# Kernel optimization log

Measured on AMD Instinct MI355X. Metric: run time of the kernel, lower is better.

The kernel has to match this reference:

```python
import jax, jax.numpy as jnp
import numpy as np

NUM_HEADS = 12


def setup_inputs() -> dict:
    key = jax.random.key(0)
    k1, k2, k3 = jax.random.split(key, 3)
    B, S, D = 2, 2048, 768
    x = jax.random.normal(k1, (B, S, D), dtype=jnp.float32)
    # torch Linear init: normal(std=0.002) weights, zero bias; stored as [in, out]
    W_qkv = jax.random.normal(k2, (D, 3 * D), dtype=jnp.float32) * 0.002
    b_qkv = jnp.zeros((3 * D,), dtype=jnp.float32)
    W_vw = jax.random.normal(k3, (D, D), dtype=jnp.float32) * 0.002
    b_vw = jnp.zeros((D,), dtype=jnp.float32)
    mask = jnp.ones((B, S), dtype=jnp.int32)  # padding mask, all valid
    return {"x": x, "W_qkv": W_qkv, "b_qkv": b_qkv, "W_vw": W_vw, "b_vw": b_vw, "mask": mask}


def reference(x, W_qkv, b_qkv, W_vw, b_vw, mask):
    B, S, D = x.shape
    H = NUM_HEADS
    Dh = D // H
    qkv = (x @ W_qkv + b_qkv).reshape(B, S, 3, H, Dh)
    q, k, v = qkv[:, :, 0], qkv[:, :, 1], qkv[:, :, 2]
    # [B, H, S, S] attention scores (full matrix, as in original)
    w = jnp.einsum('bshd,bzhd->bhsz', q, k)
    w = w / jnp.sqrt(jnp.asarray(Dh, dtype=x.dtype))  # scale=True
    # log-mask trick: padding mask [B,1,1,S] * causal tril [1,1,S,S]
    causal = jnp.tril(jnp.ones((S, S), dtype=x.dtype))
    wholemask = mask.astype(x.dtype)[:, None, None, :] * causal[None, None]
    w = w + jnp.log(wholemask)
    w = jax.nn.softmax(w, axis=-1)
    vw = jnp.einsum('bhsz,bzhd->bshd', w, v).reshape(B, S, D)
    return vw @ W_vw + b_vw
```

## Files before the change

### kernel.cpp

```cpp
#include <hip/hip_runtime.h>
#include <cmath>
#include <cstddef>

#define B_    2
#define S_    2048
#define D_    768
#define H_    12
#define DH_   64
#define NQKV_ 2304

typedef __attribute__((ext_vector_type(8))) short  short8;
typedef __attribute__((ext_vector_type(4))) float  floatx4;

__device__ __forceinline__ unsigned short f2bf(float f) {
    union { float f; unsigned u; } v; v.f = f;
    unsigned r = v.u + 0x7fffu + ((v.u >> 16) & 1u);
    return (unsigned short)(r >> 16);
}

__device__ __forceinline__ void stage16(const unsigned short* g, unsigned short* ldsbase, int lane) {
#if __has_builtin(__builtin_amdgcn_global_load_lds)
    __builtin_amdgcn_global_load_lds(
        (const __attribute__((address_space(1))) unsigned int*)g,
        (__attribute__((address_space(3))) unsigned int*)ldsbase, 16, 0, 0);
#else
    *(short8*)(ldsbase + lane * 8) = *(const short8*)g;
#endif
}

__global__ void cvt_x_kernel(const float* __restrict__ x, unsigned short* __restrict__ xb)
{
    int i = (blockIdx.x * 256 + threadIdx.x) * 8;
    float4 a = *(const float4*)(x + i);
    float4 b = *(const float4*)(x + i + 4);
    short8 v;
    v[0] = (short)f2bf(a.x); v[1] = (short)f2bf(a.y);
    v[2] = (short)f2bf(a.z); v[3] = (short)f2bf(a.w);
    v[4] = (short)f2bf(b.x); v[5] = (short)f2bf(b.y);
    v[6] = (short)f2bf(b.z); v[7] = (short)f2bf(b.w);
    *(short8*)(xb + i) = v;
}

__global__ void cvt_w_kernel(const float* __restrict__ Wq, const float* __restrict__ Wv,
                             unsigned short* __restrict__ WqT, unsigned short* __restrict__ WvT)
{
    const int z = blockIdx.z;
    const int N = z ? D_ : NQKV_;
    if ((int)blockIdx.x * 32 >= N) return;
    const float* W = z ? Wv : Wq;
    unsigned short* WT = z ? WvT : WqT;

    __shared__ float t[32][33];
    const int tx = threadIdx.x, ty = threadIdx.y;
    const int n0 = blockIdx.x * 32, k0 = blockIdx.y * 32;
    #pragma unroll
    for (int i = 0; i < 4; ++i)
        t[ty + i * 8][tx] = W[(size_t)(k0 + ty + i * 8) * N + n0 + tx];
    __syncthreads();
    #pragma unroll
    for (int i = 0; i < 4; ++i)
        WT[(size_t)(n0 + ty + i * 8) * 768 + k0 + tx] = f2bf(t[tx][ty + i * 8]);
}

__global__ void vt_kernel(const unsigned short* __restrict__ V, unsigned short* __restrict__ VT)
{
    __shared__ unsigned short t[64][72];
    const int bh = blockIdx.x, s0 = blockIdx.y * 64;
    const unsigned short* src = V + ((size_t)bh * S_ + s0) * DH_;
    const int r = threadIdx.x >> 3, c = (threadIdx.x & 7) * 8;
    #pragma unroll
    for (int it = 0; it < 2; ++it)
        *(short8*)&t[r + it * 32][c] = *(const short8*)(src + (size_t)(r + it * 32) * DH_ + c);
    __syncthreads();
    #pragma unroll
    for (int it = 0; it < 2; ++it) {
        int d = r + it * 32;
        short8 v;
        #pragma unroll
        for (int i = 0; i < 8; ++i) v[i] = (short)t[c + i][d];
        *(short8*)(VT + ((size_t)bh * DH_ + d) * S_ + s0 + c) = v;
    }
}

__global__ __launch_bounds__(256, 2)
void mm_qkv_kernel(const unsigned short* __restrict__ A, const unsigned short* __restrict__ BT,
                   const float* __restrict__ bias,
                   unsigned short* __restrict__ Qo, unsigned short* __restrict__ Ko,
                   unsigned short* __restrict__ Vo)
{
    __shared__ unsigned short As[128][32];
    __shared__ unsigned short Bs[128][32];
    const int tid = threadIdx.x;
    const int wid = tid >> 6, lane = tid & 63;
    const int q = lane >> 4, ln = lane & 15;
    const int wm = (wid & 1) * 64, wn = (wid >> 1) * 64;
    const int m0 = blockIdx.y * 128, n0 = blockIdx.x * 128;
    const int lrow = wid * 16 + (lane >> 2);
    const int lcol = (lane & 3) * 8;
    const unsigned short* Ag = A  + (size_t)(m0 + lrow) * 768 + lcol;
    const unsigned short* Bg = BT + (size_t)(n0 + lrow) * 768 + lcol;

    floatx4 acc[4][4] = {};
    for (int k0 = 0; k0 < 768; k0 += 32) {
        __syncthreads();
        stage16(Ag + k0,            &As[wid * 16][0],      lane);
        stage16(Ag + k0 + 64 * 768, &As[64 + wid * 16][0], lane);
        stage16(Bg + k0,            &Bs[wid * 16][0],      lane);
        stage16(Bg + k0 + 64 * 768, &Bs[64 + wid * 16][0], lane);
        __syncthreads();
        short8 af[4], bf[4];
        #pragma unroll
        for (int mt = 0; mt < 4; ++mt) af[mt] = *(const short8*)&As[wm + mt * 16 + ln][q * 8];
        #pragma unroll
        for (int nt = 0; nt < 4; ++nt) bf[nt] = *(const short8*)&Bs[wn + nt * 16 + ln][q * 8];
        #pragma unroll
        for (int mt = 0; mt < 4; ++mt)
            #pragma unroll
            for (int nt = 0; nt < 4; ++nt)
                acc[mt][nt] = __builtin_amdgcn_mfma_f32_16x16x32_bf16(af[mt], bf[nt], acc[mt][nt], 0, 0, 0);
    }

    const int t = n0 / 768;
    unsigned short* __restrict__ dst = (t == 0) ? Qo : ((t == 1) ? Ko : Vo);
    const int colb = n0 - t * 768 + wn;
    float bv[4];
    #pragma unroll
    for (int nt = 0; nt < 4; ++nt) bv[nt] = bias[n0 + wn + nt * 16 + ln];
    #pragma unroll
    for (int mt = 0; mt < 4; ++mt)
        #pragma unroll
        for (int r = 0; r < 4; ++r) {
            int row = m0 + wm + mt * 16 + q * 4 + r;
            int bb = row >> 11, s = row & 2047;
            #pragma unroll
            for (int nt = 0; nt < 4; ++nt) {
                int col = colb + nt * 16 + ln;
                int h = col >> 6, d = col & 63;
                dst[((size_t)(bb * H_ + h) * S_ + s) * DH_ + d] = f2bf(acc[mt][nt][r] + bv[nt]);
            }
        }
}

__global__ __launch_bounds__(256, 2)
void flash6_kernel(const unsigned short* __restrict__ Qg, const unsigned short* __restrict__ Kg,
                   const unsigned short* __restrict__ VTg, const int* __restrict__ mask,
                   unsigned short* __restrict__ VW)
{
    __shared__ unsigned short Pl[4][32][40];
    __shared__ float Ol[32][68];
    __shared__ float li_s[4][32];

    const int tid = threadIdx.x;
    const int wid = tid >> 6, lane = tid & 63;
    const int q = lane >> 4, ln = lane & 15;
    const int bh = blockIdx.x % 24;
    const int qt = 63 - blockIdx.x / 24;
    const int b = bh / H_, h = bh % H_;
    const int r0 = qt * 32;

    const unsigned short* Qb = Qg  + (size_t)bh * S_ * DH_;
    const unsigned short* Kb = Kg  + (size_t)bh * S_ * DH_;
    const unsigned short* Vt = VTg + (size_t)bh * DH_ * S_;
    const int* mb = mask + b * S_;

    short8 qf[2][2];
    #pragma unroll
    for (int mt = 0; mt < 2; ++mt)
        #pragma unroll
        for (int kk = 0; kk < 2; ++kk)
            qf[mt][kk] = *(const short8*)(Qb + (size_t)(r0 + mt * 16 + ln) * DH_ + kk * 32 + q * 8);

    floatx4 o[2][4] = {};
    float li[2][4] = {};
    const float SC = 0.125f * 1.4426950408889634f;
    const int T = qt + 1;

    for (int t = wid; t < T; t += 4) {
        const int z0 = t * 32;

        short8 kb[2][2];
        #pragma unroll
        for (int nt = 0; nt < 2; ++nt)
            #pragma unroll
            for (int kk = 0; kk < 2; ++kk)
                kb[nt][kk] = *(const short8*)(Kb + (size_t)(z0 + nt * 16 + ln) * DH_ + kk * 32 + q * 8);

        floatx4 s[2][2] = {};
        #pragma unroll
        for (int mt = 0; mt < 2; ++mt)
            #pragma unroll
            for (int nt = 0; nt < 2; ++nt) {
                s[mt][nt] = __builtin_amdgcn_mfma_f32_16x16x32_bf16(qf[mt][0], kb[nt][0], s[mt][nt], 0, 0, 0);
                s[mt][nt] = __builtin_amdgcn_mfma_f32_16x16x32_bf16(qf[mt][1], kb[nt][1], s[mt][nt], 0, 0, 0);
            }

        short8 vb[4];
        #pragma unroll
        for (int dt = 0; dt < 4; ++dt)
            vb[dt] = *(const short8*)(Vt + (size_t)(dt * 16 + ln) * S_ + z0 + q * 8);

        float mv[2];
        #pragma unroll
        for (int nt = 0; nt < 2; ++nt) mv[nt] = mb[z0 + nt * 16 + ln] ? 1.0f : 0.0f;

        const bool diag = (z0 + 31 > r0);
        #pragma unroll
        for (int mt = 0; mt < 2; ++mt)
            #pragma unroll
            for (int nt = 0; nt < 2; ++nt) {
                int z = z0 + nt * 16 + ln;
                #pragma unroll
                for (int r = 0; r < 4; ++r) {
                    float p = exp2f(s[mt][nt][r] * SC) * mv[nt];
                    if (diag) {
                        int row = r0 + mt * 16 + q * 4 + r;
                        if (z > row) p = 0.0f;
                    }
                    li[mt][r] += p;
                    Pl[wid][mt * 16 + q * 4 + r][nt * 16 + ln] = f2bf(p);
                }
            }

        #pragma unroll
        for (int mt = 0; mt < 2; ++mt) {
            short8 a = *(const short8*)&Pl[wid][mt * 16 + ln][q * 8];
            #pragma unroll
            for (int dt = 0; dt < 4; ++dt)
                o[mt][dt] = __builtin_amdgcn_mfma_f32_16x16x32_bf16(a, vb[dt], o[mt][dt], 0, 0, 0);
        }
    }

    #pragma unroll
    for (int mt = 0; mt < 2; ++mt)
        #pragma unroll
        for (int r = 0; r < 4; ++r) {
            float v = li[mt][r];
            v += __shfl_xor(v, 1);
            v += __shfl_xor(v, 2);
            v += __shfl_xor(v, 4);
            v += __shfl_xor(v, 8);
            li[mt][r] = v;
        }

    #pragma unroll
    for (int w = 0; w < 4; ++w) {
        if (wid == w) {
            #pragma unroll
            for (int mt = 0; mt < 2; ++mt)
                #pragma unroll
                for (int r = 0; r < 4; ++r) {
                    int row = mt * 16 + q * 4 + r;
                    #pragma unroll
                    for (int dt = 0; dt < 4; ++dt) {
                        if (w == 0) Ol[row][dt * 16 + ln]  = o[mt][dt][r];
                        else        Ol[row][dt * 16 + ln] += o[mt][dt][r];
                    }
                    if (ln == 0) li_s[w][row] = li[mt][r];
                }
        }
        __syncthreads();
    }

    {
        int row = tid >> 3, c = (tid & 7) * 8;
        float inv = 1.0f / (li_s[0][row] + li_s[1][row] + li_s[2][row] + li_s[3][row]);
        short8 ov;
        #pragma unroll
        for (int i = 0; i < 8; ++i) ov[i] = (short)f2bf(Ol[row][c + i] * inv);
        *(short8*)(VW + ((size_t)b * S_ + r0 + row) * D_ + h * DH_ + c) = ov;
    }
}

__global__ __launch_bounds__(256, 2)
void mm_proj_kernel(const unsigned short* __restrict__ A, const unsigned short* __restrict__ BT,
                    const float* __restrict__ bias, float* __restrict__ C)
{
    __shared__ unsigned short As[128][32];
    __shared__ unsigned short Bs[64][32];
    const int tid = threadIdx.x;
    const int wid = tid >> 6, lane = tid & 63;
    const int q = lane >> 4, ln = lane & 15;
    const int wm = (wid & 1) * 64, wn = (wid >> 1) * 32;
    const int m0 = blockIdx.y * 128, n0 = blockIdx.x * 64;
    const int lrow = wid * 16 + (lane >> 2);
    const int lcol = (lane & 3) * 8;
    const unsigned short* Ag = A  + (size_t)(m0 + lrow) * 768 + lcol;
    const unsigned short* Bg = BT + (size_t)(n0 + lrow) * 768 + lcol;

    floatx4 acc[4][2] = {};
    for (int k0 = 0; k0 < 768; k0 += 32) {
        __syncthreads();
        stage16(Ag + k0,            &As[wid * 16][0],      lane);
        stage16(Ag + k0 + 64 * 768, &As[64 + wid * 16][0], lane);
        stage16(Bg + k0,            &Bs[wid * 16][0],      lane);
        __syncthreads();
        short8 af[4], bf[2];
        #pragma unroll
        for (int mt = 0; mt < 4; ++mt) af[mt] = *(const short8*)&As[wm + mt * 16 + ln][q * 8];
        #pragma unroll
        for (int nt = 0; nt < 2; ++nt) bf[nt] = *(const short8*)&Bs[wn + nt * 16 + ln][q * 8];
        #pragma unroll
        for (int mt = 0; mt < 4; ++mt)
            #pragma unroll
            for (int nt = 0; nt < 2; ++nt)
                acc[mt][nt] = __builtin_amdgcn_mfma_f32_16x16x32_bf16(af[mt], bf[nt], acc[mt][nt], 0, 0, 0);
    }

    float bv[2];
    #pragma unroll
    for (int nt = 0; nt < 2; ++nt) bv[nt] = bias[n0 + wn + nt * 16 + ln];
    #pragma unroll
    for (int mt = 0; mt < 4; ++mt)
        #pragma unroll
        for (int r = 0; r < 4; ++r) {
            size_t row = (size_t)m0 + wm + mt * 16 + q * 4 + r;
            #pragma unroll
            for (int nt = 0; nt < 2; ++nt)
                C[row * D_ + n0 + wn + nt * 16 + ln] = acc[mt][nt][r] + bv[nt];
        }
}

extern "C" void kernel_launch(void* const* d_in, const int* in_sizes, int n_in,
                              void* d_out, int out_size, void* d_ws, size_t ws_size,
                              hipStream_t stream)
{
    (void)in_sizes; (void)n_in; (void)out_size; (void)ws_size;
    const float* x    = (const float*)d_in[0];
    const float* Wqkv = (const float*)d_in[1];
    const float* bqkv = (const float*)d_in[2];
    const float* Wvw  = (const float*)d_in[3];
    const float* bvw  = (const float*)d_in[4];
    const int*   mask = (const int*)d_in[5];
    float* out = (float*)d_out;

    const size_t XN  = (size_t)B_ * S_ * D_;
    unsigned short* ws  = (unsigned short*)d_ws;
    unsigned short* xb  = ws;
    unsigned short* WqT = xb  + XN;
    unsigned short* WvT = WqT + (size_t)NQKV_ * D_;
    unsigned short* Qb  = WvT + (size_t)D_ * D_;
    unsigned short* Kb  = Qb + XN;
    unsigned short* Vb  = Kb + XN;
    unsigned short* VbT = Vb + XN;
    unsigned short* VW  = VbT + XN;

    cvt_x_kernel<<<dim3(XN / (256 * 8)), 256, 0, stream>>>(x, xb);
    cvt_w_kernel<<<dim3(NQKV_ / 32, D_ / 32, 2), dim3(32, 8), 0, stream>>>(Wqkv, Wvw, WqT, WvT);
    mm_qkv_kernel<<<dim3(NQKV_ / 128, (B_ * S_) / 128), 256, 0, stream>>>(xb, WqT, bqkv, Qb, Kb, Vb);
    vt_kernel<<<dim3(B_ * H_, S_ / 64), 256, 0, stream>>>(Vb, VbT);
    flash6_kernel<<<dim3(24 * 64), 256, 0, stream>>>(Qb, Kb, VbT, mask, VW);
    mm_proj_kernel<<<dim3(D_ / 64, (B_ * S_) / 128), 256, 0, stream>>>(VW, WvT, bvw, out);
}
```

Baseline: 187.9 us.

## Pair causal query tiles per block, fold softmax scale into Q, add fast path

The attention kernel now processes two query tiles per block (tile i and tile 63-i), so every block does the same amount of causal work and the grid is halved. The softmax scale times log2(e) is folded into Q at the QKV projection epilogue, which removes a multiply per score. A fast path skips the per-element mask and causal checks for fully valid off-diagonal tiles, s_setprio hints are placed around the MFMA groups, and f2bf now uses the HIP bf16 intrinsic. Halving the grid leaves fewer blocks to hide latency, and rounding Q after scaling changes numerics slightly.

```diff
diff --git a/kernel.cpp b/kernel.cpp
--- a/kernel.cpp
+++ b/kernel.cpp
@@ -1,4 +1,5 @@
 #include <hip/hip_runtime.h>
+#include <hip/hip_bf16.h>
 #include <cmath>
 #include <cstddef>
 
@@ -13,9 +14,9 @@
 typedef __attribute__((ext_vector_type(4))) float  floatx4;
 
 __device__ __forceinline__ unsigned short f2bf(float f) {
-    union { float f; unsigned u; } v; v.f = f;
-    unsigned r = v.u + 0x7fffu + ((v.u >> 16) & 1u);
-    return (unsigned short)(r >> 16);
+    union { __hip_bfloat16 h; unsigned short u; } cv;
+    cv.h = __float2bfloat16(f);
+    return cv.u;
 }
 
 __device__ __forceinline__ void stage16(const unsigned short* g, unsigned short* ldsbase, int lane) {
@@ -122,6 +123,7 @@
 
     const int t = n0 / 768;
     unsigned short* __restrict__ dst = (t == 0) ? Qo : ((t == 1) ? Ko : Vo);
+    const float qscale = (t == 0) ? 0.18033688011112042f : 1.0f;
     const int colb = n0 - t * 768 + wn;
     float bv[4];
     #pragma unroll
@@ -136,13 +138,13 @@
             for (int nt = 0; nt < 4; ++nt) {
                 int col = colb + nt * 16 + ln;
                 int h = col >> 6, d = col & 63;
-                dst[((size_t)(bb * H_ + h) * S_ + s) * DH_ + d] = f2bf(acc[mt][nt][r] + bv[nt]);
+                dst[((size_t)(bb * H_ + h) * S_ + s) * DH_ + d] = f2bf((acc[mt][nt][r] + bv[nt]) * qscale);
             }
         }
 }
 
 __global__ __launch_bounds__(256, 2)
-void flash6_kernel(const unsigned short* __restrict__ Qg, const unsigned short* __restrict__ Kg,
+void flash8_kernel(const unsigned short* __restrict__ Qg, const unsigned short* __restrict__ Kg,
                    const unsigned short* __restrict__ VTg, const int* __restrict__ mask,
                    unsigned short* __restrict__ VW)
 {
@@ -154,120 +156,143 @@
     const int wid = tid >> 6, lane = tid & 63;
     const int q = lane >> 4, ln = lane & 15;
     const int bh = blockIdx.x % 24;
-    const int qt = 63 - blockIdx.x / 24;
+    const int pix = blockIdx.x / 24;
     const int b = bh / H_, h = bh % H_;
-    const int r0 = qt * 32;
 
     const unsigned short* Qb = Qg  + (size_t)bh * S_ * DH_;
     const unsigned short* Kb = Kg  + (size_t)bh * S_ * DH_;
     const unsigned short* Vt = VTg + (size_t)bh * DH_ * S_;
     const int* mb = mask + b * S_;
 
-    short8 qf[2][2];
-    #pragma unroll
-    for (int mt = 0; mt < 2; ++mt)
-        #pragma unroll
-        for (int kk = 0; kk < 2; ++kk)
-            qf[mt][kk] = *(const short8*)(Qb + (size_t)(r0 + mt * 16 + ln) * DH_ + kk * 32 + q * 8);
-
-    floatx4 o[2][4] = {};
-    float li[2][4] = {};
-    const float SC = 0.125f * 1.4426950408889634f;
-    const int T = qt + 1;
-
-    for (int t = wid; t < T; t += 4) {
-        const int z0 = t * 32;
-
-        short8 kb[2][2];
-        #pragma unroll
-        for (int nt = 0; nt < 2; ++nt)
+    for (int half = 0; half < 2; ++half) {
+        const int qt = half ? (63 - pix) : pix;
+        const int r0 = qt * 32;
+        const int T = qt + 1;
+
+        short8 qf[2][2];
+        #pragma unroll
+        for (int mt = 0; mt < 2; ++mt)
             #pragma unroll
             for (int kk = 0; kk < 2; ++kk)
-                kb[nt][kk] = *(const short8*)(Kb + (size_t)(z0 + nt * 16 + ln) * DH_ + kk * 32 + q * 8);
-
-        floatx4 s[2][2] = {};
+                qf[mt][kk] = *(const short8*)(Qb + (size_t)(r0 + mt * 16 + ln) * DH_ + kk * 32 + q * 8);
+
+        floatx4 o[2][4] = {};
+        float li[2][4] = {};
+
+        for (int t = wid; t < T; t += 4) {
+            const int z0 = t * 32;
+
+            short8 kb[2][2];
+            #pragma unroll
+            for (int nt = 0; nt < 2; ++nt)
+                #pragma unroll
+                for (int kk = 0; kk < 2; ++kk)
+                    kb[nt][kk] = *(const short8*)(Kb + (size_t)(z0 + nt * 16 + ln) * DH_ + kk * 32 + q * 8);
+
+            short8 vb[4];
+            #pragma unroll
+            for (int dt = 0; dt < 4; ++dt)
+                vb[dt] = *(const short8*)(Vt + (size_t)(dt * 16 + ln) * S_ + z0 + q * 8);
+
+            const int m0i = mb[z0 + ln];
+            const int m1i = mb[z0 + 16 + ln];
+
+            floatx4 s[2][2] = {};
+            __builtin_amdgcn_s_setprio(1);
+            #pragma unroll
+            for (int mt = 0; mt < 2; ++mt)
+                #pragma unroll
+                for (int nt = 0; nt < 2; ++nt) {
+                    s[mt][nt] = __builtin_amdgcn_mfma_f32_16x16x32_bf16(qf[mt][0], kb[nt][0], s[mt][nt], 0, 0, 0);
+                    s[mt][nt] = __builtin_amdgcn_mfma_f32_16x16x32_bf16(qf[mt][1], kb[nt][1], s[mt][nt], 0, 0, 0);
+                }
+            __builtin_amdgcn_s_setprio(0);
+
+            const bool diag = (z0 + 31 > r0);
+            if (__all(m0i && m1i) && !diag) {
+                #pragma unroll
+                for (int mt = 0; mt < 2; ++mt)
+                    #pragma unroll
+                    for (int nt = 0; nt < 2; ++nt)
+                        #pragma unroll
+                        for (int r = 0; r < 4; ++r) {
+                            float p = exp2f(s[mt][nt][r]);
+                            li[mt][r] += p;
+                            Pl[wid][mt * 16 + q * 4 + r][nt * 16 + ln] = f2bf(p);
+                        }
+            } else {
+                float mv[2];
+                mv[0] = m0i ? 1.0f : 0.0f;
+                mv[1] = m1i ? 1.0f : 0.0f;
+                #pragma unroll
+                for (int mt = 0; mt < 2; ++mt)
+                    #pragma unroll
+                    for (int nt = 0; nt < 2; ++nt) {
+                        int z = z0 + nt * 16 + ln;
+                        #pragma unroll
+                        for (int r = 0; r < 4; ++r) {
+                            float p = exp2f(s[mt][nt][r]) * mv[nt];
+                            if (diag) {
+                                int row = r0 + mt * 16 + q * 4 + r;
+                                if (z > row) p = 0.0f;
+                            }
+                            li[mt][r] += p;
+                            Pl[wid][mt * 16 + q * 4 + r][nt * 16 + ln] = f2bf(p);
+                        }
+                    }
+            }
+
+            #pragma unroll
+            for (int mt = 0; mt < 2; ++mt) {
+                short8 a = *(const short8*)&Pl[wid][mt * 16 + ln][q * 8];
+                __builtin_amdgcn_s_setprio(1);
+                #pragma unroll
+                for (int dt = 0; dt < 4; ++dt)
+                    o[mt][dt] = __builtin_amdgcn_mfma_f32_16x16x32_bf16(a, vb[dt], o[mt][dt], 0, 0, 0);
+                __builtin_amdgcn_s_setprio(0);
+            }
+        }
+
         #pragma unroll
         for (int mt = 0; mt < 2; ++mt)
             #pragma unroll
-            for (int nt = 0; nt < 2; ++nt) {
-                s[mt][nt] = __builtin_amdgcn_mfma_f32_16x16x32_bf16(qf[mt][0], kb[nt][0], s[mt][nt], 0, 0, 0);
-                s[mt][nt] = __builtin_amdgcn_mfma_f32_16x16x32_bf16(qf[mt][1], kb[nt][1], s[mt][nt], 0, 0, 0);
-            }
-
-        short8 vb[4];
-        #pragma unroll
-        for (int dt = 0; dt < 4; ++dt)
-            vb[dt] = *(const short8*)(Vt + (size_t)(dt * 16 + ln) * S_ + z0 + q * 8);
-
-        float mv[2];
-        #pragma unroll
-        for (int nt = 0; nt < 2; ++nt) mv[nt] = mb[z0 + nt * 16 + ln] ? 1.0f : 0.0f;
-
-        const bool diag = (z0 + 31 > r0);
-        #pragma unroll
-        for (int mt = 0; mt < 2; ++mt)
-            #pragma unroll
-            for (int nt = 0; nt < 2; ++nt) {
-                int z = z0 + nt * 16 + ln;
-                #pragma unroll
-                for (int r = 0; r < 4; ++r) {
-                    float p = exp2f(s[mt][nt][r] * SC) * mv[nt];
-                    if (diag) {
-                        int row = r0 + mt * 16 + q * 4 + r;
-                        if (z > row) p = 0.0f;
+            for (int r = 0; r < 4; ++r) {
+                float v = li[mt][r];
+                v += __shfl_xor(v, 1);
+                v += __shfl_xor(v, 2);
+                v += __shfl_xor(v, 4);
+                v += __shfl_xor(v, 8);
+                li[mt][r] = v;
+            }
+
+        #pragma unroll
+        for (int w = 0; w < 4; ++w) {
+            if (wid == w) {
+                #pragma unroll
+                for (int mt = 0; mt < 2; ++mt)
+                    #pragma unroll
+                    for (int r = 0; r < 4; ++r) {
+                        int row = mt * 16 + q * 4 + r;
+                        #pragma unroll
+                        for (int dt = 0; dt < 4; ++dt) {
+                            if (w == 0) Ol[row][dt * 16 + ln]  = o[mt][dt][r];
+                            else        Ol[row][dt * 16 + ln] += o[mt][dt][r];
+                        }
+                        if (ln == 0) li_s[w][row] = li[mt][r];
                     }
-                    li[mt][r] += p;
-                    Pl[wid][mt * 16 + q * 4 + r][nt * 16 + ln] = f2bf(p);
-                }
-            }
-
-        #pragma unroll
-        for (int mt = 0; mt < 2; ++mt) {
-            short8 a = *(const short8*)&Pl[wid][mt * 16 + ln][q * 8];
-            #pragma unroll
-            for (int dt = 0; dt < 4; ++dt)
-                o[mt][dt] = __builtin_amdgcn_mfma_f32_16x16x32_bf16(a, vb[dt], o[mt][dt], 0, 0, 0);
-        }
-    }
-
-    #pragma unroll
-    for (int mt = 0; mt < 2; ++mt)
-        #pragma unroll
-        for (int r = 0; r < 4; ++r) {
-            float v = li[mt][r];
-            v += __shfl_xor(v, 1);
-            v += __shfl_xor(v, 2);
-            v += __shfl_xor(v, 4);
-            v += __shfl_xor(v, 8);
-            li[mt][r] = v;
-        }
-
-    #pragma unroll
-    for (int w = 0; w < 4; ++w) {
-        if (wid == w) {
-            #pragma unroll
-            for (int mt = 0; mt < 2; ++mt)
-                #pragma unroll
-                for (int r = 0; r < 4; ++r) {
-                    int row = mt * 16 + q * 4 + r;
-                    #pragma unroll
-                    for (int dt = 0; dt < 4; ++dt) {
-                        if (w == 0) Ol[row][dt * 16 + ln]  = o[mt][dt][r];
-                        else        Ol[row][dt * 16 + ln] += o[mt][dt][r];
-                    }
-                    if (ln == 0) li_s[w][row] = li[mt][r];
-                }
-        }
-        __syncthreads();
-    }
-
-    {
-        int row = tid >> 3, c = (tid & 7) * 8;
-        float inv = 1.0f / (li_s[0][row] + li_s[1][row] + li_s[2][row] + li_s[3][row]);
-        short8 ov;
-        #pragma unroll
-        for (int i = 0; i < 8; ++i) ov[i] = (short)f2bf(Ol[row][c + i] * inv);
-        *(short8*)(VW + ((size_t)b * S_ + r0 + row) * D_ + h * DH_ + c) = ov;
+            }
+            __syncthreads();
+        }
+
+        {
+            int row = tid >> 3, c = (tid & 7) * 8;
+            float inv = 1.0f / (li_s[0][row] + li_s[1][row] + li_s[2][row] + li_s[3][row]);
+            short8 ov;
+            #pragma unroll
+            for (int i = 0; i < 8; ++i) ov[i] = (short)f2bf(Ol[row][c + i] * inv);
+            *(short8*)(VW + ((size_t)b * S_ + r0 + row) * D_ + h * DH_ + c) = ov;
+        }
+        __syncthreads();
     }
 }
 
@@ -348,6 +373,6 @@
     cvt_w_kernel<<<dim3(NQKV_ / 32, D_ / 32, 2), dim3(32, 8), 0, stream>>>(Wqkv, Wvw, WqT, WvT);
     mm_qkv_kernel<<<dim3(NQKV_ / 128, (B_ * S_) / 128), 256, 0, stream>>>(xb, WqT, bqkv, Qb, Kb, Vb);
     vt_kernel<<<dim3(B_ * H_, S_ / 64), 256, 0, stream>>>(Vb, VbT);
-    flash6_kernel<<<dim3(24 * 64), 256, 0, stream>>>(Qb, Kb, VbT, mask, VW);
+    flash8_kernel<<<dim3(24 * 32), 256, 0, stream>>>(Qb, Kb, VbT, mask, VW);
     mm_proj_kernel<<<dim3(D_ / 64, (B_ * S_) / 128), 256, 0, stream>>>(VW, WvT, bvw, out);
 }
```

New measurement: 178.9 us. 1.05x faster.
